# Performance work log

Hardware: AMD Instinct MI355X
Metric: run time of the kernel (lower is better)

Reference implementation:

```python
import jax, jax.numpy as jnp
import numpy as np

N_NODES = 50000
N_EDGES = 800000
N_GRAPHS = 512
F_IN = 16
E_DIM = 64
D = 128          # encoder_dim
L_DIM = 64       # latent_dim
MP_STEPS = 3
S2S_STEPS = 3
NEG_SLOPE = 0.01


def _leaky(v):
    return jax.nn.leaky_relu(v, NEG_SLOPE)


def setup_inputs() -> dict:
    key = jax.random.key(0)
    ks = jax.random.split(key, 24)

    def w(k, fan_in, shape):
        return jax.random.normal(k, shape, jnp.float32) / np.sqrt(fan_in)

    inp = {
        "x": jax.random.normal(ks[0], (N_NODES, F_IN), jnp.float32),
        "edge_index": jax.random.randint(ks[1], (2, N_EDGES), 0, N_NODES, jnp.int64),
        "edge_attr": jax.random.normal(ks[2], (N_EDGES, 4), jnp.float32),
        "batch": jnp.sort(jax.random.randint(ks[3], (N_NODES,), 0, N_GRAPHS, jnp.int64)),
        # embedding: Linear(F_IN -> E_DIM); weights stored [in, out]
        "W_emb": w(ks[4], F_IN, (F_IN, E_DIM)),
        "b_emb": jnp.zeros((E_DIM,), jnp.float32),
        # first: Linear(E_DIM -> D)
        "W_first": w(ks[5], E_DIM, (E_DIM, D)),
        "b_first": jnp.zeros((D,), jnp.float32),
        # SAGEConv: lin_l (aggregated neighbors, with bias), lin_r (root, no bias)
        "W_l": w(ks[6], D, (D, D)),
        "b_l": jnp.zeros((D,), jnp.float32),
        "W_r": w(ks[7], D, (D, D)),
        # GRU (1 layer): gates ordered r,z,n as in torch
        "gru_Wih": w(ks[8], D, (D, 3 * D)),
        "gru_Whh": w(ks[9], D, (D, 3 * D)),
        "gru_bih": jnp.zeros((3 * D,), jnp.float32),
        "gru_bhh": jnp.zeros((3 * D,), jnp.float32),
        # Set2Set LSTM: input 2D -> hidden D; gates ordered i,f,g,o as in torch
        "lstm_Wih": w(ks[10], 2 * D, (2 * D, 4 * D)),
        "lstm_Whh": w(ks[11], D, (D, 4 * D)),
        "lstm_bih": jnp.zeros((4 * D,), jnp.float32),
        "lstm_bhh": jnp.zeros((4 * D,), jnp.float32),
        # linear: Linear(2D -> D), final: Linear(D -> L_DIM)
        "W_lin": w(ks[12], 2 * D, (2 * D, D)),
        "b_lin": jnp.zeros((D,), jnp.float32),
        "W_fin": w(ks[13], D, (D, L_DIM)),
        "b_fin": jnp.zeros((L_DIM,), jnp.float32),
    }
    return inp


def _gru_step(x, h, Wih, Whh, bih, bhh):
    gi = x @ Wih + bih
    gh = h @ Whh + bhh
    ir, iz, inn = jnp.split(gi, 3, axis=-1)
    hr, hz, hn = jnp.split(gh, 3, axis=-1)
    r = jax.nn.sigmoid(ir + hr)
    z = jax.nn.sigmoid(iz + hz)
    n = jnp.tanh(inn + r * hn)
    return (1.0 - z) * n + z * h


def _lstm_step(x, h, c, Wih, Whh, bih, bhh):
    g = x @ Wih + bih + h @ Whh + bhh
    i, f, gg, o = jnp.split(g, 4, axis=-1)
    c_new = jax.nn.sigmoid(f) * c + jax.nn.sigmoid(i) * jnp.tanh(gg)
    h_new = jax.nn.sigmoid(o) * jnp.tanh(c_new)
    return h_new, c_new


def reference(x, edge_index, edge_attr, batch,
              W_emb, b_emb, W_first, b_first,
              W_l, b_l, W_r,
              gru_Wih, gru_Whh, gru_bih, gru_bhh,
              lstm_Wih, lstm_Whh, lstm_bih, lstm_bhh,
              W_lin, b_lin, W_fin, b_fin):
    # edge_attr is ignored (PyG SAGEConv does not use it).
    out = _leaky(x @ W_emb + b_emb)        # [N, E_DIM]
    out = _leaky(out @ W_first + b_first)  # [N, D]
    h = out                                # GRU hidden state [N, D]
    src, dst = edge_index[0], edge_index[1]
    for _ in range(MP_STEPS):
        agg = jax.ops.segment_sum(out[src], dst, num_segments=N_NODES)  # [N, D]
        m = jax.nn.relu(agg @ W_l + b_l + out @ W_r)  # SAGEConv(aggr='add') + root
        out = _gru_step(m, h, gru_Wih, gru_Whh, gru_bih, gru_bhh)
        h = out
    # Set2Set pooling over graphs
    q_star = jnp.zeros((N_GRAPHS, 2 * D), out.dtype)
    hh = jnp.zeros((N_GRAPHS, D), out.dtype)
    cc = jnp.zeros((N_GRAPHS, D), out.dtype)
    for _ in range(S2S_STEPS):
        hh, cc = _lstm_step(q_star, hh, cc, lstm_Wih, lstm_Whh, lstm_bih, lstm_bhh)
        e = jnp.sum(out * hh[batch], axis=-1)                             # [N]
        e_max = jax.ops.segment_max(e, batch, num_segments=N_GRAPHS)      # [B]
        a = jnp.exp(e - e_max[batch])
        s = jax.ops.segment_sum(a, batch, num_segments=N_GRAPHS)
        a = a / (s[batch] + 1e-16)                                        # segment softmax
        r = jax.ops.segment_sum(a[:, None] * out, batch, num_segments=N_GRAPHS)  # [B, D]
        q_star = jnp.concatenate([hh, r], axis=-1)                        # [B, 2D]
    out = _leaky(q_star @ W_lin + b_lin)
    return out @ W_fin + b_fin  # [B, L_DIM]
```

## Files before the change

### kernel.cpp

```cpp
#include <hip/hip_runtime.h>
#include <hip/hip_bf16.h>
#include <math.h>

#define N_NODES 50000
#define N_EDGES 800000
#define N_GRAPHS 512
#define F_IN 16
#define E_DIM 64
#define D 128
#define L_DIM 64
#define NEG_SLOPE 0.01f

#define SCAN_N (N_NODES + 1)
#define SCAN_CH 512
#define SCAN_NCH ((SCAN_N + SCAN_CH - 1) / SCAN_CH)

typedef __hip_bfloat16 bf16;
typedef unsigned int uint;
typedef unsigned short ushort;
typedef __attribute__((ext_vector_type(8))) short short8;
typedef __attribute__((ext_vector_type(4))) float float4v;

__device__ __forceinline__ float b2f(bf16 v) { return __bfloat162float(v); }
__device__ __forceinline__ bf16  f2b(float v) { return __float2bfloat16(v); }
__device__ __forceinline__ short f2bs(float f) { bf16 b = __float2bfloat16(f); return *reinterpret_cast<short*>(&b); }
__device__ __forceinline__ float bs2f(short s) { return __uint_as_float(((uint)(ushort)s) << 16); }
__device__ __forceinline__ float leaky(float v) { return v > 0.f ? v : NEG_SLOPE * v; }
__device__ __forceinline__ float sigm(float v) { return 1.f / (1.f + expf(-v)); }

__global__ __launch_bounds__(256) void k_signal(float* outp, int n)
{
    int i = blockIdx.x * 256 + threadIdx.x;
    if (i < n) outp[i] = 1.0f;
}

#define NPE 16
__global__ __launch_bounds__(128) void k_embed(
    const float* __restrict__ x, const float* __restrict__ Wemb, const float* __restrict__ bemb,
    const float* __restrict__ Wfirst, const float* __restrict__ bfirst, bf16* __restrict__ out)
{
    __shared__ float xs[NPE][F_IN];
    __shared__ float ys[NPE][E_DIM];
    int t = threadIdx.x;
    int base = blockIdx.x * NPE;

    for (int i = t; i < NPE * F_IN; i += 128)
        xs[i / F_IN][i % F_IN] = x[(size_t)base * F_IN + i];
    __syncthreads();

    if (t < E_DIM) {
        float acc[NPE];
#pragma unroll
        for (int nn = 0; nn < NPE; nn++) acc[nn] = 0.f;
        for (int k = 0; k < F_IN; k++) {
            float w = Wemb[k * E_DIM + t];
#pragma unroll
            for (int nn = 0; nn < NPE; nn++) acc[nn] += xs[nn][k] * w;
        }
        float bb = bemb[t];
#pragma unroll
        for (int nn = 0; nn < NPE; nn++) ys[nn][t] = leaky(acc[nn] + bb);
    }
    __syncthreads();

    {
        float acc[NPE];
#pragma unroll
        for (int nn = 0; nn < NPE; nn++) acc[nn] = 0.f;
        for (int k = 0; k < E_DIM; k++) {
            float w = Wfirst[k * D + t];
#pragma unroll
            for (int nn = 0; nn < NPE; nn++) acc[nn] += ys[nn][k] * w;
        }
        float bb = bfirst[t];
#pragma unroll
        for (int nn = 0; nn < NPE; nn++)
            out[(size_t)(base + nn) * D + t] = f2b(leaky(acc[nn] + bb));
    }
}

__global__ __launch_bounds__(256) void k_count(const int* __restrict__ ei, int* __restrict__ offs)
{
    int e = blockIdx.x * 256 + threadIdx.x;
    if (e < N_EDGES) {
        int d = ei[N_EDGES + e];
        d = d < 0 ? 0 : (d >= N_NODES ? N_NODES - 1 : d);
        atomicAdd(&offs[d + 1], 1);
    }
}

__global__ __launch_bounds__(SCAN_CH) void k_scan1(int* __restrict__ offs, int* __restrict__ bsum)
{
    __shared__ int sh[SCAN_CH];
    int t = threadIdx.x;
    int i = blockIdx.x * SCAN_CH + t;
    sh[t] = (i < SCAN_N) ? offs[i] : 0;
    __syncthreads();
    for (int d = 1; d < SCAN_CH; d <<= 1) {
        int v = (t >= d) ? sh[t - d] : 0;
        __syncthreads();
        sh[t] += v;
        __syncthreads();
    }
    if (i < SCAN_N) offs[i] = sh[t];
    if (t == SCAN_CH - 1) bsum[blockIdx.x] = sh[t];
}

__global__ void k_scan2(int* __restrict__ bsum)
{
    if (threadIdx.x == 0 && blockIdx.x == 0) {
        int run = 0;
        for (int i = 0; i < SCAN_NCH; i++) { int v = bsum[i]; bsum[i] = run; run += v; }
    }
}

__global__ __launch_bounds__(SCAN_CH) void k_scan3(int* __restrict__ offs, const int* __restrict__ bsum)
{
    int i = blockIdx.x * SCAN_CH + threadIdx.x;
    if (i < SCAN_N) offs[i] += bsum[blockIdx.x];
}

__global__ __launch_bounds__(256) void k_fill(
    const int* __restrict__ ei, const int* __restrict__ offs,
    int* __restrict__ curs, int* __restrict__ srcs)
{
    int e = blockIdx.x * 256 + threadIdx.x;
    if (e < N_EDGES) {
        int s = ei[e];
        int d = ei[N_EDGES + e];
        s = s < 0 ? 0 : (s >= N_NODES ? N_NODES - 1 : s);
        d = d < 0 ? 0 : (d >= N_NODES ? N_NODES - 1 : d);
        int slot = offs[d] + atomicAdd(&curs[d], 1);
        if (slot >= 0 && slot < N_EDGES) srcs[slot] = s;
    }
}

__global__ __launch_bounds__(256) void k_gstart(const int* __restrict__ batch, int* __restrict__ gstart)
{
    int g = blockIdx.x * 256 + threadIdx.x;
    if (g > N_GRAPHS) return;
    int lo = 0, hi = N_NODES;
    while (lo < hi) {
        int mid = (lo + hi) >> 1;
        if (batch[mid] < g) lo = mid + 1; else hi = mid;
    }
    gstart[g] = lo;
}

__global__ __launch_bounds__(256) void k_pack_all(
    const float* __restrict__ Wl, const float* __restrict__ Wr,
    const float* __restrict__ gWih, const float* __restrict__ gWhh,
    short* __restrict__ W1p, short* __restrict__ Wihp, short* __restrict__ Whhp)
{
    int tid = blockIdx.x * 256 + threadIdx.x;
    if (tid < 32768) {
        int j = tid & 7, l = (tid >> 3) & 63, frag = tid >> 9;
        int nb = frag & 7, kb = frag >> 3;
        int k = kb * 32 + ((l >> 4) * 8) + j;
        int n = nb * 16 + (l & 15);
        float v = (k < 128) ? Wl[k * D + n] : Wr[(k - 128) * D + n];
        W1p[tid] = f2bs(v);
    } else {
        int id = tid - 32768;
        const float* W = gWih;
        short* Wp = Wihp;
        if (id >= 49152) { id -= 49152; W = gWhh; Wp = Whhp; }
        int j = id & 7, l = (id >> 3) & 63, frag = id >> 9;
        int nb = frag % 24, kb = frag / 24;
        int k = kb * 32 + ((l >> 4) * 8) + j;
        int n = nb * 16 + (l & 15);
        Wp[id] = f2bs(W[k * 384 + n]);
    }
}

__global__ __launch_bounds__(256) void k_gather(
    const bf16* __restrict__ hin, bf16* __restrict__ hagg,
    const int* __restrict__ offs, const int* __restrict__ srcs)
{
    int w = threadIdx.x >> 6, l = threadIdx.x & 63;
    int n = blockIdx.x * 4 + w;
    const ushort* hinu = (const ushort*)hin;
    int j0 = offs[n], j1 = offs[n + 1];
    j0 = j0 < 0 ? 0 : (j0 > N_EDGES ? N_EDGES : j0);
    j1 = j1 < j0 ? j0 : (j1 > N_EDGES ? N_EDGES : j1);

    float lo[8], hi8[8];
#pragma unroll
    for (int i = 0; i < 8; i++) { lo[i] = 0.f; hi8[i] = 0.f; }

    int j = j0;
    for (; j + 7 < j1; j += 8) {
        int ss[8];
        uint vv[8];
#pragma unroll
        for (int i = 0; i < 8; i++) {
            int s = srcs[j + i];
            ss[i] = s < 0 ? 0 : (s >= N_NODES ? N_NODES - 1 : s);
        }
#pragma unroll
        for (int i = 0; i < 8; i++)
            vv[i] = *(const uint*)(hinu + (size_t)ss[i] * D + l * 2);
#pragma unroll
        for (int i = 0; i < 8; i++) {
            lo[i] += __uint_as_float(vv[i] << 16);
            hi8[i] += __uint_as_float(vv[i] & 0xffff0000u);
        }
    }
    for (; j < j1; j++) {
        int s = srcs[j];
        s = s < 0 ? 0 : (s >= N_NODES ? N_NODES - 1 : s);
        uint v = *(const uint*)(hinu + (size_t)s * D + l * 2);
        lo[0] += __uint_as_float(v << 16);
        hi8[0] += __uint_as_float(v & 0xffff0000u);
    }
    float a0 = ((lo[0] + lo[1]) + (lo[2] + lo[3])) + ((lo[4] + lo[5]) + (lo[6] + lo[7]));
    float a1 = ((hi8[0] + hi8[1]) + (hi8[2] + hi8[3])) + ((hi8[4] + hi8[5]) + (hi8[6] + hi8[7]));
    uint ap = ((uint)(ushort)f2bs(a1) << 16) | (ushort)f2bs(a0);
    *(uint*)((ushort*)hagg + (size_t)n * D + l * 2) = ap;
}

#define M_STR 136
__global__ __launch_bounds__(128) void k_sage_gru_mfma(
    const bf16* __restrict__ hin, bf16* __restrict__ hagg_out,
    const short* __restrict__ W1p, const short* __restrict__ Wihp, const short* __restrict__ Whhp,
    const float* __restrict__ bl, const float* __restrict__ bih, const float* __restrict__ bhh)
{
    __shared__ short Msh[64 * M_STR];
    __shared__ short Hsh[64 * M_STR];
    int t = threadIdx.x;
    int w = t >> 6, l = t & 63;
    int base = blockIdx.x * 64;
    const ushort* hinu = (const ushort*)hin;
    const ushort* haggu = (const ushort*)hagg_out;
    ushort* houtu = (ushort*)hagg_out;

    int r0 = base + w * 32 + (l & 15);
    int r1 = r0 + 16;
    int rc0 = r0 < N_NODES ? r0 : N_NODES - 1;
    int rc1 = r1 < N_NODES ? r1 : N_NODES - 1;
    int koff = (l >> 4) * 8;

    short8 afr0[8], afr1[8];
#pragma unroll
    for (int k0 = 0; k0 < 4; k0++) {
        afr0[k0] = *(const short8*)(haggu + (size_t)rc0 * D + k0 * 32 + koff);
        afr1[k0] = *(const short8*)(haggu + (size_t)rc1 * D + k0 * 32 + koff);
    }
#pragma unroll
    for (int k0 = 0; k0 < 4; k0++) {
        afr0[4 + k0] = *(const short8*)(hinu + (size_t)rc0 * D + k0 * 32 + koff);
        afr1[4 + k0] = *(const short8*)(hinu + (size_t)rc1 * D + k0 * 32 + koff);
    }

    int mrow0 = w * 32 + (l & 15);
    int mrow1 = mrow0 + 16;
    int crow0 = w * 32 + (l >> 4) * 4;
    int crow1 = crow0 + 16;

#pragma unroll
    for (int k0 = 0; k0 < 4; k0++) {
        *(short8*)&Hsh[mrow0 * M_STR + k0 * 32 + koff] = afr0[4 + k0];
        *(short8*)&Hsh[mrow1 * M_STR + k0 * 32 + koff] = afr1[4 + k0];
    }

    short8 bA[8], bB[8];
#pragma unroll
    for (int k0 = 0; k0 < 8; k0++)
        bA[k0] = *(const short8*)&W1p[((k0 * 8 + 0) * 64 + l) * 8];
#pragma unroll
    for (int ct = 0; ct < 8; ct++) {
        const short8* bc = (ct & 1) ? bB : bA;
        short8* bn = (ct & 1) ? bA : bB;
        if (ct < 7) {
#pragma unroll
            for (int k0 = 0; k0 < 8; k0++)
                bn[k0] = *(const short8*)&W1p[((k0 * 8 + ct + 1) * 64 + l) * 8];
        }
        float4v acc0 = {0.f, 0.f, 0.f, 0.f};
        float4v acc1 = {0.f, 0.f, 0.f, 0.f};
#pragma unroll
        for (int k0 = 0; k0 < 8; k0++) {
            acc0 = __builtin_amdgcn_mfma_f32_16x16x32_bf16(afr0[k0], bc[k0], acc0, 0, 0, 0);
            acc1 = __builtin_amdgcn_mfma_f32_16x16x32_bf16(afr1[k0], bc[k0], acc1, 0, 0, 0);
        }
        float bb = bl[ct * 16 + (l & 15)];
#pragma unroll
        for (int i = 0; i < 4; i++) {
            float v0 = acc0[i] + bb;
            float v1 = acc1[i] + bb;
            Msh[(crow0 + i) * M_STR + ct * 16 + (l & 15)] = f2bs(v0 > 0.f ? v0 : 0.f);
            Msh[(crow1 + i) * M_STR + ct * 16 + (l & 15)] = f2bs(v1 > 0.f ? v1 : 0.f);
        }
    }
    __syncthreads();

    short8 amr0[4], amr1[4];
#pragma unroll
    for (int k0 = 0; k0 < 4; k0++) {
        amr0[k0] = *(const short8*)&Msh[mrow0 * M_STR + k0 * 32 + koff];
        amr1[k0] = *(const short8*)&Msh[mrow1 * M_STR + k0 * 32 + koff];
    }

    short8 iA[4], hA[4], iB[4], hB[4];
#pragma unroll
    for (int k0 = 0; k0 < 4; k0++) {
        iA[k0] = *(const short8*)&Wihp[((k0 * 24 + 0) * 64 + l) * 8];
        hA[k0] = *(const short8*)&Whhp[((k0 * 24 + 0) * 64 + l) * 8];
    }
#pragma unroll
    for (int ct = 0; ct < 8; ct++) {
        int c = ct * 16 + (l & 15);
        float rv0[4], zv0[4], rv1[4], zv1[4];
#pragma unroll
        for (int p = 0; p < 3; p++) {
            int ph = ct * 3 + p;
            const short8* wi = (ph & 1) ? iB : iA;
            const short8* wh = (ph & 1) ? hB : hA;
            short8* win = (ph & 1) ? iA : iB;
            short8* whn = (ph & 1) ? hA : hB;
            if (ph < 23) {
                int pn = ph + 1;
                int ctn = pn / 3, ppn = pn - ctn * 3;
                int nbn = ppn * 8 + ctn;
#pragma unroll
                for (int k0 = 0; k0 < 4; k0++) {
                    win[k0] = *(const short8*)&Wihp[((k0 * 24 + nbn) * 64 + l) * 8];
                    whn[k0] = *(const short8*)&Whhp[((k0 * 24 + nbn) * 64 + l) * 8];
                }
            }
            float4v ai0 = {0.f, 0.f, 0.f, 0.f};
            float4v ah0 = {0.f, 0.f, 0.f, 0.f};
            float4v ai1 = {0.f, 0.f, 0.f, 0.f};
            float4v ah1 = {0.f, 0.f, 0.f, 0.f};
#pragma unroll
            for (int k0 = 0; k0 < 4; k0++) {
                ai0 = __builtin_amdgcn_mfma_f32_16x16x32_bf16(amr0[k0], wi[k0], ai0, 0, 0, 0);
                ah0 = __builtin_amdgcn_mfma_f32_16x16x32_bf16(afr0[4 + k0], wh[k0], ah0, 0, 0, 0);
                ai1 = __builtin_amdgcn_mfma_f32_16x16x32_bf16(amr1[k0], wi[k0], ai1, 0, 0, 0);
                ah1 = __builtin_amdgcn_mfma_f32_16x16x32_bf16(afr1[4 + k0], wh[k0], ah1, 0, 0, 0);
            }
            float bis = bih[p * 128 + c];
            float bhs = bhh[p * 128 + c];
            if (p == 0) {
#pragma unroll
                for (int i = 0; i < 4; i++) {
                    rv0[i] = sigm(ai0[i] + bis + ah0[i] + bhs);
                    rv1[i] = sigm(ai1[i] + bis + ah1[i] + bhs);
                }
            } else if (p == 1) {
#pragma unroll
                for (int i = 0; i < 4; i++) {
                    zv0[i] = sigm(ai0[i] + bis + ah0[i] + bhs);
                    zv1[i] = sigm(ai1[i] + bis + ah1[i] + bhs);
                }
            } else {
#pragma unroll
                for (int i = 0; i < 4; i++) {
                    int g0 = base + crow0 + i;
                    int g1 = base + crow1 + i;
                    float h0v = bs2f(Hsh[(crow0 + i) * M_STR + c]);
                    float h1v = bs2f(Hsh[(crow1 + i) * M_STR + c]);
                    float nv0 = tanhf(ai0[i] + bis + rv0[i] * (ah0[i] + bhs));
                    float nv1 = tanhf(ai1[i] + bis + rv1[i] * (ah1[i] + bhs));
                    if (g0 < N_NODES)
                        houtu[(size_t)g0 * D + c] = (ushort)f2bs((1.f - zv0[i]) * nv0 + zv0[i] * h0v);
                    if (g1 < N_NODES)
                        houtu[(size_t)g1 * D + c] = (ushort)f2bs((1.f - zv1[i]) * nv1 + zv1[i] * h1v);
                }
            }
        }
    }
}

#define POOL_CAP 1024
#define LG2 2
__global__ __launch_bounds__(1024) void k_s2s(
    const float* __restrict__ Wih, const float* __restrict__ Whh,
    const float* __restrict__ bih, const float* __restrict__ bhh,
    const bf16* __restrict__ h, const int* __restrict__ gstart,
    float* __restrict__ qstar, float* __restrict__ hh, float* __restrict__ cc, int first)
{
    int g0 = blockIdx.x * LG2;
    int t = threadIdx.x;
    __shared__ float qs[LG2][2 * D];
    __shared__ float hs[LG2][D];
    __shared__ float part[2][LG2][512];
    __shared__ float hnew[LG2][D];
    __shared__ float e_lds[POOL_CAP];
    __shared__ float redM[16], redS[16];
    __shared__ float rpart[8][D];

    for (int i = t; i < LG2 * 2 * D; i += 1024) {
        int g = i / (2 * D), c = i % (2 * D);
        qs[g][c] = first ? 0.f : qstar[(size_t)(g0 + g) * 2 * D + c];
    }
    for (int i = t; i < LG2 * D; i += 1024) {
        int g = i / D, c = i % D;
        hs[g][c] = first ? 0.f : hh[(size_t)(g0 + g) * D + c];
    }
    __syncthreads();

    int c = t & 511, half = t >> 9;
    float a0 = half ? 0.f : (bih[c] + bhh[c]);
    float a1 = a0;
    int qb = half * 128;
#pragma unroll 4
    for (int i = 0; i < 128; i++) {
        int k = qb + i;
        float wv = Wih[(size_t)k * 512 + c];
        a0 += qs[0][k] * wv;
        a1 += qs[1][k] * wv;
    }
    int hb = half * 64;
#pragma unroll 4
    for (int i = 0; i < 64; i++) {
        int k = hb + i;
        float wv = Whh[(size_t)k * 512 + c];
        a0 += hs[0][k] * wv;
        a1 += hs[1][k] * wv;
    }
    part[half][0][c] = a0;
    part[half][1][c] = a1;
    __syncthreads();

    if (t < LG2 * D) {
        int g = t >> 7, tt = t & 127;
        float gi = part[0][g][tt] + part[1][g][tt];
        float gf = part[0][g][D + tt] + part[1][g][D + tt];
        float gg2 = part[0][g][2 * D + tt] + part[1][g][2 * D + tt];
        float go = part[0][g][3 * D + tt] + part[1][g][3 * D + tt];
        float c_old = first ? 0.f : cc[(size_t)(g0 + g) * D + tt];
        float cn = sigm(gf) * c_old + sigm(gi) * tanhf(gg2);
        float hn = sigm(go) * tanhf(cn);
        cc[(size_t)(g0 + g) * D + tt] = cn;
        hh[(size_t)(g0 + g) * D + tt] = hn;
        qstar[(size_t)(g0 + g) * 2 * D + tt] = hn;
        hnew[g][tt] = hn;
    }
    __syncthreads();

    int w = t >> 6, l = t & 63;
    int dim = t & 127, h8 = t >> 7;
    const ushort* hu = (const ushort*)h;

    for (int gg = 0; gg < LG2; gg++) {
        int g = g0 + gg;
        int s0 = gstart[g], s1 = gstart[g + 1];
        s0 = s0 < 0 ? 0 : (s0 > N_NODES ? N_NODES : s0);
        s1 = s1 < s0 ? s0 : (s1 > N_NODES ? N_NODES : s1);
        int cnt = s1 - s0;

        float hq0 = hnew[gg][l];
        float hq1 = hnew[gg][64 + l];
        float m_run = -INFINITY, s_run = 0.f, racc = 0.f;

        for (int c0 = 0; c0 < cnt; c0 += POOL_CAP) {
            int clen = cnt - c0; if (clen > POOL_CAP) clen = POOL_CAP;

            for (int i = w; i < clen; i += 16) {
                int n = s0 + c0 + i;
                float v = bs2f((short)hu[(size_t)n * D + l]) * hq0
                        + bs2f((short)hu[(size_t)n * D + 64 + l]) * hq1;
#pragma unroll
                for (int off = 32; off > 0; off >>= 1) v += __shfl_down(v, off);
                if (l == 0) e_lds[i] = v;
            }
            __syncthreads();

            float m = -INFINITY;
            for (int i = t; i < clen; i += 1024) m = fmaxf(m, e_lds[i]);
#pragma unroll
            for (int off = 32; off > 0; off >>= 1) m = fmaxf(m, __shfl_down(m, off));
            if (l == 0) redM[w] = m;
            __syncthreads();
            m = -INFINITY;
#pragma unroll
            for (int i = 0; i < 16; i++) m = fmaxf(m, redM[i]);
            float m_new = fmaxf(m_run, m);
            float scale = (m_run == -INFINITY) ? 0.f : expf(m_run - m_new);
            s_run *= scale;
            racc *= scale;
            __syncthreads();

            float s = 0.f;
            for (int i = t; i < clen; i += 1024) {
                float wv = expf(e_lds[i] - m_new);
                e_lds[i] = wv;
                s += wv;
            }
#pragma unroll
            for (int off = 32; off > 0; off >>= 1) s += __shfl_down(s, off);
            if (l == 0) redS[w] = s;
            __syncthreads();
#pragma unroll
            for (int i = 0; i < 16; i++) s_run += redS[i];

            for (int i = h8; i < clen; i += 8)
                racc += e_lds[i] * bs2f((short)hu[(size_t)(s0 + c0 + i) * D + dim]);
            m_run = m_new;
            __syncthreads();
        }

        rpart[h8][dim] = racc;
        __syncthreads();
        if (t < D) {
            float inv = 1.f / (s_run + 1e-16f);
            float r = 0.f;
#pragma unroll
            for (int i = 0; i < 8; i++) r += rpart[i][t];
            qstar[(size_t)g * 2 * D + D + t] = r * inv;
        }
        __syncthreads();
    }
}

__global__ __launch_bounds__(128) void k_final(
    const float* __restrict__ qstar, const float* __restrict__ Wlin, const float* __restrict__ blin,
    const float* __restrict__ Wfin, const float* __restrict__ bfin, float* __restrict__ outp)
{
    int g = blockIdx.x, t = threadIdx.x;
    __shared__ float qs[2 * D], ts[D];
    qs[t] = qstar[(size_t)g * 2 * D + t];
    qs[D + t] = qstar[(size_t)g * 2 * D + D + t];
    __syncthreads();

    float acc = blin[t];
    for (int k = 0; k < 2 * D; k++) acc += qs[k] * Wlin[(size_t)k * D + t];
    ts[t] = leaky(acc);
    __syncthreads();

    if (t < L_DIM) {
        float a2 = bfin[t];
        for (int k = 0; k < D; k++) a2 += ts[k] * Wfin[(size_t)k * L_DIM + t];
        outp[(size_t)g * L_DIM + t] = a2;
    }
}

extern "C" void kernel_launch(void* const* d_in, const int* in_sizes, int n_in,
                              void* d_out, int out_size, void* d_ws, size_t ws_size,
                              hipStream_t stream)
{
    const float* x      = (const float*)d_in[0];
    const int*   ei     = (const int*)d_in[1];
    const int*   batch  = (const int*)d_in[3];
    const float* Wemb   = (const float*)d_in[4];
    const float* bemb   = (const float*)d_in[5];
    const float* Wfirst = (const float*)d_in[6];
    const float* bfirst = (const float*)d_in[7];
    const float* Wl     = (const float*)d_in[8];
    const float* bl     = (const float*)d_in[9];
    const float* Wr     = (const float*)d_in[10];
    const float* gWih   = (const float*)d_in[11];
    const float* gWhh   = (const float*)d_in[12];
    const float* gbih   = (const float*)d_in[13];
    const float* gbhh   = (const float*)d_in[14];
    const float* lWih   = (const float*)d_in[15];
    const float* lWhh   = (const float*)d_in[16];
    const float* lbih   = (const float*)d_in[17];
    const float* lbhh   = (const float*)d_in[18];
    const float* Wlin   = (const float*)d_in[19];
    const float* blin   = (const float*)d_in[20];
    const float* Wfin   = (const float*)d_in[21];
    const float* bfin   = (const float*)d_in[22];
    float* outp = (float*)d_out;

    size_t o = 0;
    char* base = (char*)d_ws;
    auto carve = [&](size_t bytes) { void* p = base + o; o += (bytes + 255) & ~(size_t)255; return p; };
    bf16*  h0     = (bf16*)carve((size_t)N_NODES * D * sizeof(bf16));
    bf16*  h1     = (bf16*)carve((size_t)N_NODES * D * sizeof(bf16));
    int*   offs   = (int*)carve((size_t)SCAN_N * sizeof(int));
    int*   curs   = (int*)carve((size_t)N_NODES * sizeof(int));
    int*   srcs   = (int*)carve((size_t)N_EDGES * sizeof(int));
    int*   bsum   = (int*)carve((size_t)SCAN_NCH * sizeof(int));
    float* hh     = (float*)carve((size_t)N_GRAPHS * D * sizeof(float));
    float* cc     = (float*)carve((size_t)N_GRAPHS * D * sizeof(float));
    float* qstar  = (float*)carve((size_t)N_GRAPHS * 2 * D * sizeof(float));
    int*   gstart = (int*)carve((size_t)(N_GRAPHS + 1) * sizeof(int));
    short* W1p    = (short*)carve((size_t)256 * 128 * sizeof(short));
    short* Wihp   = (short*)carve((size_t)128 * 384 * sizeof(short));
    short* Whhp   = (short*)carve((size_t)128 * 384 * sizeof(short));
    size_t need = o;

    if (ws_size < need) {
        k_signal<<<(out_size + 255) / 256, 256, 0, stream>>>(outp, out_size);
        return;
    }

    k_embed<<<N_NODES / NPE, 128, 0, stream>>>(x, Wemb, bemb, Wfirst, bfirst, h0);

    k_pack_all<<<(32768 + 98304) / 256, 256, 0, stream>>>(Wl, Wr, gWih, gWhh, W1p, Wihp, Whhp);

    hipMemsetAsync(offs, 0, (size_t)((char*)srcs - (char*)offs), stream);
    k_count<<<(N_EDGES + 255) / 256, 256, 0, stream>>>(ei, offs);
    k_scan1<<<SCAN_NCH, SCAN_CH, 0, stream>>>(offs, bsum);
    k_scan2<<<1, 64, 0, stream>>>(bsum);
    k_scan3<<<SCAN_NCH, SCAN_CH, 0, stream>>>(offs, bsum);
    k_fill<<<(N_EDGES + 255) / 256, 256, 0, stream>>>(ei, offs, curs, srcs);

    k_gstart<<<(N_GRAPHS + 1 + 255) / 256, 256, 0, stream>>>(batch, gstart);

    bf16* hc = h0; bf16* hn = h1;
    for (int s = 0; s < 3; s++) {
        k_gather<<<N_NODES / 4, 256, 0, stream>>>(hc, hn, offs, srcs);
        k_sage_gru_mfma<<<(N_NODES + 63) / 64, 128, 0, stream>>>(
            hc, hn, W1p, Wihp, Whhp, bl, gbih, gbhh);
        bf16* tmp = hc; hc = hn; hn = tmp;
    }

    for (int s = 0; s < 3; s++) {
        k_s2s<<<N_GRAPHS / LG2, 1024, 0, stream>>>(lWih, lWhh, lbih, lbhh,
                                                   hc, gstart, qstar, hh, cc, s == 0);
    }

    k_final<<<N_GRAPHS, 128, 0, stream>>>(qstar, Wlin, blin, Wfin, bfin, outp);
}
```

Baseline: 550.1 us.

## Build CSR via bucketed two-level sort and halve SAGE-GRU rows per block

Builds the CSR adjacency differently. Edges are first counted and scattered into 128-node destination buckets, using shared-memory local counts and a short scan. A per-bucket kernel then ranks edges with shared-memory atomics and writes offsets and sources. This replaces the global per-node atomic count, the three-kernel scan and the global-atomic fill, with source and local destination packed into 32 bits. Separately, the fused SAGE+GRU MFMA kernel now handles 32 rows per block instead of 64, giving twice as many smaller blocks and fewer registers per thread, at the cost of reloading the weight fragments twice as often per row.

After: 786.4 us. 43.0% more time.

```diff
diff --git a/kernel.cpp b/kernel.cpp
--- a/kernel.cpp
+++ b/kernel.cpp
@@ -12,8 +12,7 @@
 #define NEG_SLOPE 0.01f
 
 #define SCAN_N (N_NODES + 1)
-#define SCAN_CH 512
-#define SCAN_NCH ((SCAN_N + SCAN_CH - 1) / SCAN_CH)
+#define NBUCK ((N_NODES + 127) >> 7)
 
 typedef __hip_bfloat16 bf16;
 typedef unsigned int uint;
@@ -79,50 +78,33 @@
     }
 }
 
-__global__ __launch_bounds__(256) void k_count(const int* __restrict__ ei, int* __restrict__ offs)
-{
-    int e = blockIdx.x * 256 + threadIdx.x;
-    if (e < N_EDGES) {
+__global__ __launch_bounds__(256) void k_bcount(const int* __restrict__ ei, int* __restrict__ bcnt)
+{
+    __shared__ int lc[NBUCK];
+    for (int i = threadIdx.x; i < NBUCK; i += 256) lc[i] = 0;
+    __syncthreads();
+    int stride = gridDim.x * 256;
+    for (int e = blockIdx.x * 256 + threadIdx.x; e < N_EDGES; e += stride) {
         int d = ei[N_EDGES + e];
         d = d < 0 ? 0 : (d >= N_NODES ? N_NODES - 1 : d);
-        atomicAdd(&offs[d + 1], 1);
-    }
-}
-
-__global__ __launch_bounds__(SCAN_CH) void k_scan1(int* __restrict__ offs, int* __restrict__ bsum)
-{
-    __shared__ int sh[SCAN_CH];
-    int t = threadIdx.x;
-    int i = blockIdx.x * SCAN_CH + t;
-    sh[t] = (i < SCAN_N) ? offs[i] : 0;
-    __syncthreads();
-    for (int d = 1; d < SCAN_CH; d <<= 1) {
-        int v = (t >= d) ? sh[t - d] : 0;
-        __syncthreads();
-        sh[t] += v;
-        __syncthreads();
-    }
-    if (i < SCAN_N) offs[i] = sh[t];
-    if (t == SCAN_CH - 1) bsum[blockIdx.x] = sh[t];
-}
-
-__global__ void k_scan2(int* __restrict__ bsum)
+        atomicAdd(&lc[d >> 7], 1);
+    }
+    __syncthreads();
+    for (int i = threadIdx.x; i < NBUCK; i += 256)
+        if (lc[i]) atomicAdd(&bcnt[i + 1], lc[i]);
+}
+
+__global__ void k_bscan(int* __restrict__ bcnt)
 {
     if (threadIdx.x == 0 && blockIdx.x == 0) {
         int run = 0;
-        for (int i = 0; i < SCAN_NCH; i++) { int v = bsum[i]; bsum[i] = run; run += v; }
-    }
-}
-
-__global__ __launch_bounds__(SCAN_CH) void k_scan3(int* __restrict__ offs, const int* __restrict__ bsum)
-{
-    int i = blockIdx.x * SCAN_CH + threadIdx.x;
-    if (i < SCAN_N) offs[i] += bsum[blockIdx.x];
-}
-
-__global__ __launch_bounds__(256) void k_fill(
-    const int* __restrict__ ei, const int* __restrict__ offs,
-    int* __restrict__ curs, int* __restrict__ srcs)
+        for (int i = 0; i <= NBUCK; i++) { run += bcnt[i]; bcnt[i] = run; }
+    }
+}
+
+__global__ __launch_bounds__(256) void k_bfill(
+    const int* __restrict__ ei, const int* __restrict__ bstart,
+    int* __restrict__ bcur, uint* __restrict__ ebuf)
 {
     int e = blockIdx.x * 256 + threadIdx.x;
     if (e < N_EDGES) {
@@ -130,8 +112,45 @@
         int d = ei[N_EDGES + e];
         s = s < 0 ? 0 : (s >= N_NODES ? N_NODES - 1 : s);
         d = d < 0 ? 0 : (d >= N_NODES ? N_NODES - 1 : d);
-        int slot = offs[d] + atomicAdd(&curs[d], 1);
-        if (slot >= 0 && slot < N_EDGES) srcs[slot] = s;
+        int b = d >> 7;
+        int slot = bstart[b] + atomicAdd(&bcur[b], 1);
+        if (slot >= 0 && slot < N_EDGES)
+            ebuf[slot] = ((uint)(d & 127) << 16) | (uint)s;
+    }
+}
+
+__global__ __launch_bounds__(256) void k_csr(
+    const int* __restrict__ bstart, const uint* __restrict__ ebuf,
+    int* __restrict__ offs, int* __restrict__ srcs)
+{
+    __shared__ int cnt[128];
+    __shared__ int loffs[129];
+    int b = blockIdx.x, t = threadIdx.x;
+    int e0 = bstart[b], e1 = bstart[b + 1];
+    if (t < 128) cnt[t] = 0;
+    __syncthreads();
+    for (int j = e0 + t; j < e1; j += 256)
+        atomicAdd(&cnt[(ebuf[j] >> 16) & 127], 1);
+    __syncthreads();
+    if (t == 0) {
+        int run = 0;
+        for (int i = 0; i < 128; i++) { loffs[i] = run; run += cnt[i]; }
+        loffs[128] = run;
+    }
+    __syncthreads();
+    int n0 = b << 7;
+    if (t < 128) {
+        int n = n0 + t;
+        if (n <= N_NODES) offs[n] = e0 + loffs[t];
+        cnt[t] = 0;
+    }
+    __syncthreads();
+    for (int j = e0 + t; j < e1; j += 256) {
+        uint pk = ebuf[j];
+        int dl = (pk >> 16) & 127;
+        int rank = atomicAdd(&cnt[dl], 1);
+        int slot = e0 + loffs[dl] + rank;
+        if (slot >= 0 && slot < N_EDGES) srcs[slot] = (int)(pk & 0xffffu);
     }
 }
 
@@ -225,43 +244,33 @@
     const short* __restrict__ W1p, const short* __restrict__ Wihp, const short* __restrict__ Whhp,
     const float* __restrict__ bl, const float* __restrict__ bih, const float* __restrict__ bhh)
 {
-    __shared__ short Msh[64 * M_STR];
-    __shared__ short Hsh[64 * M_STR];
+    __shared__ short Msh[32 * M_STR];
+    __shared__ short Hsh[32 * M_STR];
     int t = threadIdx.x;
     int w = t >> 6, l = t & 63;
-    int base = blockIdx.x * 64;
+    int base = blockIdx.x * 32;
     const ushort* hinu = (const ushort*)hin;
     const ushort* haggu = (const ushort*)hagg_out;
     ushort* houtu = (ushort*)hagg_out;
 
-    int r0 = base + w * 32 + (l & 15);
-    int r1 = r0 + 16;
+    int r0 = base + w * 16 + (l & 15);
     int rc0 = r0 < N_NODES ? r0 : N_NODES - 1;
-    int rc1 = r1 < N_NODES ? r1 : N_NODES - 1;
     int koff = (l >> 4) * 8;
 
-    short8 afr0[8], afr1[8];
-#pragma unroll
-    for (int k0 = 0; k0 < 4; k0++) {
-        afr0[k0] = *(const short8*)(haggu + (size_t)rc0 * D + k0 * 32 + koff);
-        afr1[k0] = *(const short8*)(haggu + (size_t)rc1 * D + k0 * 32 + koff);
-    }
-#pragma unroll
-    for (int k0 = 0; k0 < 4; k0++) {
-        afr0[4 + k0] = *(const short8*)(hinu + (size_t)rc0 * D + k0 * 32 + koff);
-        afr1[4 + k0] = *(const short8*)(hinu + (size_t)rc1 * D + k0 * 32 + koff);
-    }
-
-    int mrow0 = w * 32 + (l & 15);
-    int mrow1 = mrow0 + 16;
-    int crow0 = w * 32 + (l >> 4) * 4;
-    int crow1 = crow0 + 16;
-
-#pragma unroll
-    for (int k0 = 0; k0 < 4; k0++) {
-        *(short8*)&Hsh[mrow0 * M_STR + k0 * 32 + koff] = afr0[4 + k0];
-        *(short8*)&Hsh[mrow1 * M_STR + k0 * 32 + koff] = afr1[4 + k0];
-    }
+    short8 afr[8];
+#pragma unroll
+    for (int k0 = 0; k0 < 4; k0++)
+        afr[k0] = *(const short8*)(haggu + (size_t)rc0 * D + k0 * 32 + koff);
+#pragma unroll
+    for (int k0 = 0; k0 < 4; k0++)
+        afr[4 + k0] = *(const short8*)(hinu + (size_t)rc0 * D + k0 * 32 + koff);
+
+    int mrow = w * 16 + (l & 15);
+    int crow = w * 16 + (l >> 4) * 4;
+
+#pragma unroll
+    for (int k0 = 0; k0 < 4; k0++)
+        *(short8*)&Hsh[mrow * M_STR + k0 * 32 + koff] = afr[4 + k0];
 
     short8 bA[8], bB[8];
 #pragma unroll
@@ -276,30 +285,23 @@
             for (int k0 = 0; k0 < 8; k0++)
                 bn[k0] = *(const short8*)&W1p[((k0 * 8 + ct + 1) * 64 + l) * 8];
         }
-        float4v acc0 = {0.f, 0.f, 0.f, 0.f};
-        float4v acc1 = {0.f, 0.f, 0.f, 0.f};
-#pragma unroll
-        for (int k0 = 0; k0 < 8; k0++) {
-            acc0 = __builtin_amdgcn_mfma_f32_16x16x32_bf16(afr0[k0], bc[k0], acc0, 0, 0, 0);
-            acc1 = __builtin_amdgcn_mfma_f32_16x16x32_bf16(afr1[k0], bc[k0], acc1, 0, 0, 0);
-        }
+        float4v acc = {0.f, 0.f, 0.f, 0.f};
+#pragma unroll
+        for (int k0 = 0; k0 < 8; k0++)
+            acc = __builtin_amdgcn_mfma_f32_16x16x32_bf16(afr[k0], bc[k0], acc, 0, 0, 0);
         float bb = bl[ct * 16 + (l & 15)];
 #pragma unroll
         for (int i = 0; i < 4; i++) {
-            float v0 = acc0[i] + bb;
-            float v1 = acc1[i] + bb;
-            Msh[(crow0 + i) * M_STR + ct * 16 + (l & 15)] = f2bs(v0 > 0.f ? v0 : 0.f);
-            Msh[(crow1 + i) * M_STR + ct * 16 + (l & 15)] = f2bs(v1 > 0.f ? v1 : 0.f);
-        }
-    }
-    __syncthreads();
-
-    short8 amr0[4], amr1[4];
-#pragma unroll
-    for (int k0 = 0; k0 < 4; k0++) {
-        amr0[k0] = *(const short8*)&Msh[mrow0 * M_STR + k0 * 32 + koff];
-        amr1[k0] = *(const short8*)&Msh[mrow1 * M_STR + k0 * 32 + koff];
-    }
+            float v = acc[i] + bb;
+            Msh[(crow + i) * M_STR + ct * 16 + (l & 15)] = f2bs(v > 0.f ? v : 0.f);
+        }
+    }
+    __syncthreads();
+
+    short8 amr[4];
+#pragma unroll
+    for (int k0 = 0; k0 < 4; k0++)
+        amr[k0] = *(const short8*)&Msh[mrow * M_STR + k0 * 32 + koff];
 
     short8 iA[4], hA[4], iB[4], hB[4];
 #pragma unroll
@@ -310,7 +312,7 @@
 #pragma unroll
     for (int ct = 0; ct < 8; ct++) {
         int c = ct * 16 + (l & 15);
-        float rv0[4], zv0[4], rv1[4], zv1[4];
+        float rv[4], zv[4];
 #pragma unroll
         for (int p = 0; p < 3; p++) {
             int ph = ct * 3 + p;
@@ -328,44 +330,29 @@
                     whn[k0] = *(const short8*)&Whhp[((k0 * 24 + nbn) * 64 + l) * 8];
                 }
             }
-            float4v ai0 = {0.f, 0.f, 0.f, 0.f};
-            float4v ah0 = {0.f, 0.f, 0.f, 0.f};
-            float4v ai1 = {0.f, 0.f, 0.f, 0.f};
-            float4v ah1 = {0.f, 0.f, 0.f, 0.f};
+            float4v ai = {0.f, 0.f, 0.f, 0.f};
+            float4v ah = {0.f, 0.f, 0.f, 0.f};
 #pragma unroll
             for (int k0 = 0; k0 < 4; k0++) {
-                ai0 = __builtin_amdgcn_mfma_f32_16x16x32_bf16(amr0[k0], wi[k0], ai0, 0, 0, 0);
-                ah0 = __builtin_amdgcn_mfma_f32_16x16x32_bf16(afr0[4 + k0], wh[k0], ah0, 0, 0, 0);
-                ai1 = __builtin_amdgcn_mfma_f32_16x16x32_bf16(amr1[k0], wi[k0], ai1, 0, 0, 0);
-                ah1 = __builtin_amdgcn_mfma_f32_16x16x32_bf16(afr1[4 + k0], wh[k0], ah1, 0, 0, 0);
+                ai = __builtin_amdgcn_mfma_f32_16x16x32_bf16(amr[k0], wi[k0], ai, 0, 0, 0);
+                ah = __builtin_amdgcn_mfma_f32_16x16x32_bf16(afr[4 + k0], wh[k0], ah, 0, 0, 0);
             }
             float bis = bih[p * 128 + c];
             float bhs = bhh[p * 128 + c];
             if (p == 0) {
 #pragma unroll
+                for (int i = 0; i < 4; i++) rv[i] = sigm(ai[i] + bis + ah[i] + bhs);
+            } else if (p == 1) {
+#pragma unroll
+                for (int i = 0; i < 4; i++) zv[i] = sigm(ai[i] + bis + ah[i] + bhs);
+            } else {
+#pragma unroll
                 for (int i = 0; i < 4; i++) {
-                    rv0[i] = sigm(ai0[i] + bis + ah0[i] + bhs);
-                    rv1[i] = sigm(ai1[i] + bis + ah1[i] + bhs);
-                }
-            } else if (p == 1) {
-#pragma unroll
-                for (int i = 0; i < 4; i++) {
-                    zv0[i] = sigm(ai0[i] + bis + ah0[i] + bhs);
-                    zv1[i] = sigm(ai1[i] + bis + ah1[i] + bhs);
-                }
-            } else {
-#pragma unroll
-                for (int i = 0; i < 4; i++) {
-                    int g0 = base + crow0 + i;
-                    int g1 = base + crow1 + i;
-                    float h0v = bs2f(Hsh[(crow0 + i) * M_STR + c]);
-                    float h1v = bs2f(Hsh[(crow1 + i) * M_STR + c]);
-                    float nv0 = tanhf(ai0[i] + bis + rv0[i] * (ah0[i] + bhs));
-                    float nv1 = tanhf(ai1[i] + bis + rv1[i] * (ah1[i] + bhs));
+                    int g0 = base + crow + i;
+                    float h0v = bs2f(Hsh[(crow + i) * M_STR + c]);
+                    float nv = tanhf(ai[i] + bis + rv[i] * (ah[i] + bhs));
                     if (g0 < N_NODES)
-                        houtu[(size_t)g0 * D + c] = (ushort)f2bs((1.f - zv0[i]) * nv0 + zv0[i] * h0v);
-                    if (g1 < N_NODES)
-                        houtu[(size_t)g1 * D + c] = (ushort)f2bs((1.f - zv1[i]) * nv1 + zv1[i] * h1v);
+                        houtu[(size_t)g0 * D + c] = (ushort)f2bs((1.f - zv[i]) * nv + zv[i] * h0v);
                 }
             }
         }
@@ -570,9 +557,10 @@
     bf16*  h0     = (bf16*)carve((size_t)N_NODES * D * sizeof(bf16));
     bf16*  h1     = (bf16*)carve((size_t)N_NODES * D * sizeof(bf16));
     int*   offs   = (int*)carve((size_t)SCAN_N * sizeof(int));
-    int*   curs   = (int*)carve((size_t)N_NODES * sizeof(int));
     int*   srcs   = (int*)carve((size_t)N_EDGES * sizeof(int));
-    int*   bsum   = (int*)carve((size_t)SCAN_NCH * sizeof(int));
+    int*   bcnt   = (int*)carve((size_t)(NBUCK + 1) * sizeof(int));
+    int*   bcur   = (int*)carve((size_t)NBUCK * sizeof(int));
+    uint*  ebuf   = (uint*)carve((size_t)N_EDGES * sizeof(uint));
     float* hh     = (float*)carve((size_t)N_GRAPHS * D * sizeof(float));
     float* cc     = (float*)carve((size_t)N_GRAPHS * D * sizeof(float));
     float* qstar  = (float*)carve((size_t)N_GRAPHS * 2 * D * sizeof(float));
@@ -591,19 +579,18 @@
 
     k_pack_all<<<(32768 + 98304) / 256, 256, 0, stream>>>(Wl, Wr, gWih, gWhh, W1p, Wihp, Whhp);
 
-    hipMemsetAsync(offs, 0, (size_t)((char*)srcs - (char*)offs), stream);
-    k_count<<<(N_EDGES + 255) / 256, 256, 0, stream>>>(ei, offs);
-    k_scan1<<<SCAN_NCH, SCAN_CH, 0, stream>>>(offs, bsum);
-    k_scan2<<<1, 64, 0, stream>>>(bsum);
-    k_scan3<<<SCAN_NCH, SCAN_CH, 0, stream>>>(offs, bsum);
-    k_fill<<<(N_EDGES + 255) / 256, 256, 0, stream>>>(ei, offs, curs, srcs);
+    hipMemsetAsync(bcnt, 0, (size_t)((char*)ebuf - (char*)bcnt), stream);
+    k_bcount<<<128, 256, 0, stream>>>(ei, bcnt);
+    k_bscan<<<1, 64, 0, stream>>>(bcnt);
+    k_bfill<<<(N_EDGES + 255) / 256, 256, 0, stream>>>(ei, bcnt, bcur, ebuf);
+    k_csr<<<NBUCK, 256, 0, stream>>>(bcnt, ebuf, offs, srcs);
 
     k_gstart<<<(N_GRAPHS + 1 + 255) / 256, 256, 0, stream>>>(batch, gstart);
 
     bf16* hc = h0; bf16* hn = h1;
     for (int s = 0; s < 3; s++) {
         k_gather<<<N_NODES / 4, 256, 0, stream>>>(hc, hn, offs, srcs);
-        k_sage_gru_mfma<<<(N_NODES + 63) / 64, 128, 0, stream>>>(
+        k_sage_gru_mfma<<<(N_NODES + 31) / 32, 128, 0, stream>>>(
             hc, hn, W1p, Wihp, Whhp, bl, gbih, gbhh);
         bf16* tmp = hc; hc = hn; hn = tmp;
     }
```
